# Optimization experiments

Hardware: AMD Instinct MI355X
Metric: run time of the kernel (lower is better)

The kernel has to match this reference:

```python
import jax, jax.numpy as jnp
import numpy as np

B, C, H, W = 8, 512, 64, 64
C8 = C // 8


def setup_inputs() -> dict:
    key = jax.random.key(0)
    ks = jax.random.split(key, 9)
    s = 1.0 / np.sqrt(C)
    return {
        "view1": jax.random.normal(ks[0], (B, C, H, W), jnp.float32),
        "view2": jax.random.normal(ks[1], (B, C, H, W), jnp.float32),
        "Wq": jax.random.normal(ks[2], (C8, C), jnp.float32) * s,
        "bq": jax.random.normal(ks[3], (C8,), jnp.float32) * 0.01,
        "Wk": jax.random.normal(ks[4], (C8, C), jnp.float32) * s,
        "bk": jax.random.normal(ks[5], (C8,), jnp.float32) * 0.01,
        "Wv": jax.random.normal(ks[6], (C, C), jnp.float32) * s,
        "bv": jax.random.normal(ks[7], (C,), jnp.float32) * 0.01,
        "gamma": jnp.array([0.5], jnp.float32),  # nn.Parameter(zeros(1)) in torch; nonzero here for nontrivial output
    }


def reference(view1, view2, Wq, bq, Wk, bk, Wv, bv, gamma):
    b, c, h, w = view1.shape
    n = h * w
    # 1x1 convs == per-pixel linear over channel dim
    q = jnp.einsum("bchw,oc->bohw", view1, Wq) + bq[None, :, None, None]
    k = jnp.einsum("bchw,oc->bohw", view2, Wk) + bk[None, :, None, None]
    v = jnp.einsum("bchw,oc->bohw", view2, Wv) + bv[None, :, None, None]
    q = q.reshape(b, -1, n).transpose(0, 2, 1)  # (B, N, C/8)
    k = k.reshape(b, -1, n)                      # (B, C/8, N)
    v = v.reshape(b, c, n)                       # (B, C, N)
    # no scaling, matching the original module
    attn = jax.nn.softmax(jnp.einsum("bnd,bdm->bnm", q, k), axis=-1)  # (B, N, N)
    out = jnp.einsum("bcn,bmn->bcm", v, attn).reshape(b, c, h, w)
    return gamma[0] * out + view1
```

## Files before the change

### kernel.cpp

```cpp
#include <hip/hip_runtime.h>

#define NB 8
#define NC 512
#define NPIX 4096
#define LOG2E 1.44269504088896340736f
#define C0TERM 28.853900817779268f

typedef __attribute__((ext_vector_type(4))) float f32x4;
typedef __attribute__((ext_vector_type(8))) short bf16x8;
typedef __attribute__((ext_vector_type(4))) unsigned short u16x4;

static __device__ __forceinline__ short f2bf(float f){
    union { float f; unsigned u; } v; v.f = f;
    unsigned r = v.u + 0x7fffu + ((v.u >> 16) & 1u);
    return (short)(r >> 16);
}

static __device__ __forceinline__ void gload16(const void* g, void* l){
    __builtin_amdgcn_global_load_lds(
        (const __attribute__((address_space(1))) char*)g,
        (__attribute__((address_space(3))) char*)l, 16, 0, 0);
}

__global__ void k_wconv(const float* __restrict__ wq, const float* __restrict__ wk,
                        const float* __restrict__ wv,
                        short* __restrict__ wqb, short* __restrict__ wkb,
                        short* __restrict__ wvb){
    int i = blockIdx.x * 256 + threadIdx.x;
    if (i < 64*NC){ wqb[i] = f2bf(wq[i]); wkb[i] = f2bf(wk[i]); }
    if (i < NC*NC){ wvb[i] = f2bf(wv[i]); }
}

__global__ __launch_bounds__(256) void k_projq(const float* __restrict__ X,
                                               const short* __restrict__ W,
                                               const float* __restrict__ bias,
                                               short* __restrict__ out){
    const int b = blockIdx.y;
    const int wv = threadIdx.x >> 6;
    const int lane = threadIdx.x & 63;
    const int g = lane >> 4, c16 = lane & 15;
    const int n0w = blockIdx.x * 64 + wv * 16;
    const float* Xb = X + (size_t)b * NC * NPIX;

    f32x4 acc[4];
#pragma unroll
    for (int f = 0; f < 4; ++f) acc[f] = (f32x4){0.f,0.f,0.f,0.f};

    for (int c0 = 0; c0 < NC; c0 += 32){
        bf16x8 a;
#pragma unroll
        for (int j = 0; j < 8; ++j)
            a[j] = f2bf(Xb[(size_t)(c0 + 8*g + j) * NPIX + n0w + c16]);
#pragma unroll
        for (int f = 0; f < 4; ++f){
            bf16x8 bfr = *(const bf16x8*)(W + (size_t)(f*16 + c16) * NC + c0 + 8*g);
            acc[f] = __builtin_amdgcn_mfma_f32_16x16x32_bf16(a, bfr, acc[f], 0, 0, 0);
        }
    }
#pragma unroll
    for (int f = 0; f < 4; ++f){
        int o = f*16 + c16;
        float bo = bias[o];
#pragma unroll
        for (int i = 0; i < 4; ++i)
            out[((size_t)b*NPIX + n0w + 4*g + i)*64 + o] = f2bf(acc[f][i] + bo);
    }
}

__global__ __launch_bounds__(256) void k_trans(const float* __restrict__ X,
                                               short* __restrict__ Xt){
    __shared__ __align__(16) short T[64][72];
    const int n0 = blockIdx.x * 64;
    const int c0 = blockIdx.y * 64;
    const int b  = blockIdx.z;
    const int t  = threadIdx.x;
    {
        const int cl = t >> 2;
        const int nq = (t & 3) * 16;
        const float* src = X + ((size_t)b*NC + c0 + cl)*NPIX + n0 + nq;
#pragma unroll
        for (int q = 0; q < 4; ++q){
            f32x4 v = *(const f32x4*)(src + q*4);
#pragma unroll
            for (int i = 0; i < 4; ++i)
                T[nq + q*4 + i][cl] = f2bf(v[i]);
        }
    }
    __syncthreads();
    {
        const int n  = t >> 2;
        const int cs = (t & 3) * 16;
        short* dst = Xt + ((size_t)b*NPIX + n0 + n)*NC + c0 + cs;
        *(f32x4*)dst       = *(const f32x4*)&T[n][cs];
        *(f32x4*)(dst + 8) = *(const f32x4*)&T[n][cs + 8];
    }
}

__global__ __launch_bounds__(256) void k_projv(const short* __restrict__ Xt,
                                               const short* __restrict__ W,
                                               const float* __restrict__ bias,
                                               short* __restrict__ vout){
    const int o0 = blockIdx.x * 128;
    const int n0 = blockIdx.y * 128;
    const int b  = blockIdx.z;
    const int wv = threadIdx.x >> 6;
    const int lane = threadIdx.x & 63;
    const int g = lane >> 4, c16 = lane & 15;
    const int wo = wv & 1, wn = wv >> 1;

    const short* Xb = Xt + ((size_t)b*NPIX + n0 + wn*64)*NC;
    const short* Wb = W + (size_t)(o0 + wo*64)*NC;

    f32x4 acc[4][4];
#pragma unroll
    for (int nf = 0; nf < 4; ++nf)
#pragma unroll
        for (int of = 0; of < 4; ++of) acc[nf][of] = (f32x4){0.f,0.f,0.f,0.f};

    for (int c0 = 0; c0 < NC; c0 += 32){
        bf16x8 af[4], bf_[4];
#pragma unroll
        for (int f = 0; f < 4; ++f){
            af[f]  = *(const bf16x8*)(Xb + (size_t)(f*16 + c16)*NC + c0 + 8*g);
            bf_[f] = *(const bf16x8*)(Wb + (size_t)(f*16 + c16)*NC + c0 + 8*g);
        }
#pragma unroll
        for (int nf = 0; nf < 4; ++nf)
#pragma unroll
            for (int of = 0; of < 4; ++of)
                acc[nf][of] = __builtin_amdgcn_mfma_f32_16x16x32_bf16(af[nf], bf_[of], acc[nf][of], 0,0,0);
    }

#pragma unroll
    for (int of = 0; of < 4; ++of){
        int o = o0 + wo*64 + of*16 + c16;
        float bo = bias[o];
#pragma unroll
        for (int nf = 0; nf < 4; ++nf){
            int n = n0 + wn*64 + nf*16 + 4*g;
            u16x4 pk;
#pragma unroll
            for (int i = 0; i < 4; ++i) pk[i] = (unsigned short)f2bf(acc[nf][of][i] + bo);
            *(u16x4*)(vout + ((size_t)b*NC + o)*NPIX + n) = pk;
        }
    }
}

__global__ __launch_bounds__(256) void k_projk(const short* __restrict__ Xt,
                                               const short* __restrict__ W,
                                               const float* __restrict__ bias,
                                               short* __restrict__ kout){
    const int n0 = blockIdx.x * 256;
    const int b  = blockIdx.y;
    const int wv = threadIdx.x >> 6;
    const int lane = threadIdx.x & 63;
    const int g = lane >> 4, c16 = lane & 15;

    const short* Xb = Xt + ((size_t)b*NPIX + n0 + wv*64)*NC;

    f32x4 acc[4][4];
#pragma unroll
    for (int of = 0; of < 4; ++of)
#pragma unroll
        for (int nf = 0; nf < 4; ++nf) acc[of][nf] = (f32x4){0.f,0.f,0.f,0.f};

    for (int c0 = 0; c0 < NC; c0 += 32){
        bf16x8 af[4], bf_[4];
#pragma unroll
        for (int f = 0; f < 4; ++f){
            af[f]  = *(const bf16x8*)(W + (size_t)(f*16 + c16)*NC + c0 + 8*g);
            bf_[f] = *(const bf16x8*)(Xb + (size_t)(f*16 + c16)*NC + c0 + 8*g);
        }
#pragma unroll
        for (int of = 0; of < 4; ++of)
#pragma unroll
            for (int nf = 0; nf < 4; ++nf)
                acc[of][nf] = __builtin_amdgcn_mfma_f32_16x16x32_bf16(af[of], bf_[nf], acc[of][nf], 0,0,0);
    }

#pragma unroll
    for (int nf = 0; nf < 4; ++nf){
        int n = n0 + wv*64 + nf*16 + c16;
#pragma unroll
        for (int of = 0; of < 4; ++of){
            int o = of*16 + 4*g;
            u16x4 pk;
#pragma unroll
            for (int i = 0; i < 4; ++i) pk[i] = (unsigned short)f2bf(acc[of][nf][i] + bias[o+i]);
            *(u16x4*)(kout + ((size_t)b*NPIX + n)*64 + o) = pk;
        }
    }
}

__global__ __launch_bounds__(256) void k_projkv(const float* __restrict__ X,
                                                const short* __restrict__ Wv_,
                                                const float* __restrict__ bv_,
                                                const short* __restrict__ Wk_,
                                                const float* __restrict__ bk_,
                                                short* __restrict__ vout,
                                                short* __restrict__ kout){
    const int b = blockIdx.y;
    const int wv = threadIdx.x >> 6;
    const int lane = threadIdx.x & 63;
    const int g = lane >> 4, c16 = lane & 15;
    const int n0w = blockIdx.x * 32 + (wv & 1) * 16;
    const int oh = wv >> 1;
    const int o0v = oh * 256;
    const int o0k = oh * 32;
    const float* Xb = X + (size_t)b * NC * NPIX;

    f32x4 accv[16], acck[2];
#pragma unroll
    for (int f = 0; f < 16; ++f) accv[f] = (f32x4){0.f,0.f,0.f,0.f};
#pragma unroll
    for (int f = 0; f < 2;  ++f) acck[f] = (f32x4){0.f,0.f,0.f,0.f};

    for (int c0 = 0; c0 < NC; c0 += 32){
        bf16x8 a;
#pragma unroll
        for (int j = 0; j < 8; ++j)
            a[j] = f2bf(Xb[(size_t)(c0 + 8*g + j) * NPIX + n0w + c16]);
#pragma unroll
        for (int f = 0; f < 16; ++f){
            bf16x8 bfr = *(const bf16x8*)(Wv_ + (size_t)(o0v + f*16 + c16) * NC + c0 + 8*g);
            accv[f] = __builtin_amdgcn_mfma_f32_16x16x32_bf16(a, bfr, accv[f], 0, 0, 0);
        }
#pragma unroll
        for (int f = 0; f < 2; ++f){
            bf16x8 bfr = *(const bf16x8*)(Wk_ + (size_t)(o0k + f*16 + c16) * NC + c0 + 8*g);
            acck[f] = __builtin_amdgcn_mfma_f32_16x16x32_bf16(a, bfr, acck[f], 0, 0, 0);
        }
    }
#pragma unroll
    for (int f = 0; f < 16; ++f){
        int o = o0v + f*16 + c16;
        float bo = bv_[o];
        u16x4 pk;
#pragma unroll
        for (int i = 0; i < 4; ++i) pk[i] = (unsigned short)f2bf(accv[f][i] + bo);
        *(u16x4*)(vout + ((size_t)b*NC + o)*NPIX + n0w + 4*g) = pk;
    }
#pragma unroll
    for (int f = 0; f < 2; ++f){
        int o = o0k + f*16 + c16;
        float bo = bk_[o];
#pragma unroll
        for (int i = 0; i < 4; ++i)
            kout[((size_t)b*NPIX + n0w + 4*g + i)*64 + o] = f2bf(acck[f][i] + bo);
    }
}

__global__ __launch_bounds__(256) void k_qk(const short* __restrict__ qb,
                                            const short* __restrict__ kb,
                                            short* __restrict__ P,
                                            float* __restrict__ Lpart,
                                            int b0){
    __shared__ __align__(16) short Pt[64*256];
    const int m0 = blockIdx.x * 64;
    const int n0 = blockIdx.y * 256;
    const int bz = blockIdx.z;
    const int b  = b0 + bz;
    const int wv = threadIdx.x >> 6;
    const int lane = threadIdx.x & 63;
    const int g = lane >> 4, c16 = lane & 15;
    const int nsub = wv * 64;

    bf16x8 qf[4][2];
#pragma unroll
    for (int mf = 0; mf < 4; ++mf)
#pragma unroll
        for (int kk = 0; kk < 2; ++kk)
            qf[mf][kk] = *(const bf16x8*)(qb + ((size_t)b*NPIX + m0 + mf*16 + c16)*64 + kk*32 + 8*g);

    float lsum[4] = {0.f,0.f,0.f,0.f};
    char* Ptb = (char*)Pt;

#pragma unroll
    for (int nf = 0; nf < 4; ++nf){
        bf16x8 kf0 = *(const bf16x8*)(kb + ((size_t)b*NPIX + n0 + nsub + nf*16 + c16)*64 + 8*g);
        bf16x8 kf1 = *(const bf16x8*)(kb + ((size_t)b*NPIX + n0 + nsub + nf*16 + c16)*64 + 32 + 8*g);
#pragma unroll
        for (int mf = 0; mf < 4; ++mf){
            f32x4 s = (f32x4){0.f,0.f,0.f,0.f};
            s = __builtin_amdgcn_mfma_f32_16x16x32_bf16(kf0, qf[mf][0], s, 0,0,0);
            s = __builtin_amdgcn_mfma_f32_16x16x32_bf16(kf1, qf[mf][1], s, 0,0,0);
            u16x4 pk;
#pragma unroll
            for (int i = 0; i < 4; ++i){
                float p = exp2f(fmaf(s[i], LOG2E, -C0TERM));
                lsum[mf] += p;
                pk[i] = (unsigned short)f2bf(p);
            }
            int m = mf*16 + c16;
            int ncol = nsub + nf*16 + 4*g;
            *(u16x4*)(Ptb + m*512 + ((2*ncol) ^ ((m&7)<<4))) = pk;
        }
    }
    __syncthreads();

    {
        char* Pgb = (char*)(P + ((size_t)bz*NPIX + m0)*NPIX + n0);
        const int chunk = threadIdx.x & 31;
        const int row8  = threadIdx.x >> 5;
#pragma unroll
        for (int p = 0; p < 8; ++p){
            int row = p*8 + row8;
            f32x4 v = *(const f32x4*)(Ptb + row*512 + ((chunk*16) ^ ((row&7)<<4)));
            *(f32x4*)(Pgb + (size_t)row*(NPIX*2) + chunk*16) = v;
        }
    }

#pragma unroll
    for (int mf = 0; mf < 4; ++mf){
        lsum[mf] += __shfl_xor(lsum[mf], 16);
        lsum[mf] += __shfl_xor(lsum[mf], 32);
    }
    if (lane < 16){
        size_t base = ((size_t)bz*64 + blockIdx.y*4 + wv)*NPIX + m0 + lane;
#pragma unroll
        for (int mf = 0; mf < 4; ++mf)
            Lpart[base + mf*16] = lsum[mf];
    }
}

__global__ __launch_bounds__(256) void k_lred(const float* __restrict__ Lpart,
                                              const float* __restrict__ gamma,
                                              float* __restrict__ scale){
    int idx = blockIdx.x * 256 + threadIdx.x;
    int bz = idx >> 12, m = idx & 4095;
    float s = 0.f;
    for (int sl = 0; sl < 64; ++sl)
        s += Lpart[((size_t)bz*64 + sl)*NPIX + m];
    scale[idx] = gamma[0] / s;
}

__global__ __launch_bounds__(256) void k_pv(const short* __restrict__ vb,
                                            const short* __restrict__ P,
                                            const float* __restrict__ scale,
                                            const float* __restrict__ view1,
                                            float* __restrict__ out,
                                            int b0){
    __shared__ __align__(16) short At[2][128*64];
    __shared__ __align__(16) short Bt[2][128*64];
    const int p  = blockIdx.x + 4*blockIdx.y;
    const int mt = (p & 7) | (((p >> 5) & 3) << 3);
    const int ct = (p >> 3) & 3;
    const int c0 = ct * 128;
    const int m0 = mt * 128;
    const int bz = blockIdx.z;
    const int b  = b0 + bz;
    const int wv = threadIdx.x >> 6;
    const int lane = threadIdx.x & 63;
    const int g = lane >> 4, c16 = lane & 15;
    const int wc = wv & 1, wm = wv >> 1;
    const int lrow = lane >> 3;
    const int srcg = (lane & 7) ^ lrow;
    const int swz  = (c16 & 7) << 4;

    const char* Vg = (const char*)(vb + ((size_t)b*NC + c0)*NPIX);
    const char* Pg = (const char*)(P + ((size_t)bz*NPIX + m0)*NPIX);

    f32x4 acc[4][4];
#pragma unroll
    for (int cf = 0; cf < 4; ++cf)
#pragma unroll
        for (int mf = 0; mf < 4; ++mf) acc[cf][mf] = (f32x4){0.f,0.f,0.f,0.f};

    auto stage = [&](int buf, int t){
        size_t nbyte = (size_t)t * 64 * 2;
#pragma unroll
        for (int j = 0; j < 4; ++j){
            int r0 = wv*32 + j*8;
            int row = r0 + lrow;
            gload16(Vg + (size_t)row*(NPIX*2) + nbyte + srcg*16, (char*)&At[buf][0] + r0*128);
            gload16(Pg + (size_t)row*(NPIX*2) + nbyte + srcg*16, (char*)&Bt[buf][0] + r0*128);
        }
    };

    stage(0, 0);
    __syncthreads();

    for (int t = 0; t < 64; ++t){
        int buf = t & 1;
        if (t < 63) stage(buf ^ 1, t + 1);
        const char* A  = (const char*)&At[buf][0];
        const char* Bp = (const char*)&Bt[buf][0];
#pragma unroll
        for (int kk = 0; kk < 2; ++kk){
            bf16x8 af[4], bfm[4];
#pragma unroll
            for (int f = 0; f < 4; ++f){
                af[f]  = *(const bf16x8*)(A  + (wc*64 + f*16 + c16)*128 + ((kk*64 + g*16) ^ swz));
                bfm[f] = *(const bf16x8*)(Bp + (wm*64 + f*16 + c16)*128 + ((kk*64 + g*16) ^ swz));
            }
#pragma unroll
            for (int cf = 0; cf < 4; ++cf)
#pragma unroll
                for (int mf = 0; mf < 4; ++mf)
                    acc[cf][mf] = __builtin_amdgcn_mfma_f32_16x16x32_bf16(af[cf], bfm[mf], acc[cf][mf], 0,0,0);
        }
        __syncthreads();
    }

    float sc[4];
#pragma unroll
    for (int mf = 0; mf < 4; ++mf)
        sc[mf] = scale[(size_t)bz*NPIX + m0 + wm*64 + mf*16 + c16];
#pragma unroll
    for (int cf = 0; cf < 4; ++cf){
#pragma unroll
        for (int mf = 0; mf < 4; ++mf){
            int m = m0 + wm*64 + mf*16 + c16;
#pragma unroll
            for (int i = 0; i < 4; ++i){
                int c = c0 + wc*64 + cf*16 + 4*g + i;
                size_t idx = ((size_t)b*NC + c)*NPIX + m;
                out[idx] = sc[mf]*acc[cf][mf][i] + view1[idx];
            }
        }
    }
}

__global__ __launch_bounds__(512, 2) void k_attn(const short* __restrict__ qb,
                                                 const short* __restrict__ kb,
                                                 const short* __restrict__ vb,
                                                 const float* __restrict__ view1,
                                                 const float* __restrict__ gamma,
                                                 float* __restrict__ out){
    __shared__ __align__(16) short P[2][64*64];
    __shared__ float Lred[128];

    const int bid = blockIdx.x;
    const int b  = bid & 7;
    const int m0 = (bid >> 3) * 64;
    const int wv = threadIdx.x >> 6;
    const int lane = threadIdx.x & 63;
    const int g = lane >> 4, c16 = lane & 15;
    const int msubA = (wv & 3) * 16;
    const int nhalf = wv >> 2;
    const int c0w = wv * 64;

    const short* qrow = qb + ((size_t)b*NPIX + m0 + msubA + c16)*64 + 8*g;
    bf16x8 qa0 = *(const bf16x8*)qrow;
    bf16x8 qa1 = *(const bf16x8*)(qrow + 32);

    const size_t kbase = (size_t)b * NPIX * 64;
    const int mrow = msubA + c16;
    const int swz = (mrow & 7) << 4;
    float Lacc = 0.f;

    f32x4 acc[4][4];
#pragma unroll
    for (int f = 0; f < 4; ++f)
#pragma unroll
        for (int cf = 0; cf < 4; ++cf) acc[f][cf] = (f32x4){0.f,0.f,0.f,0.f};

    char* Pb0 = (char*)&P[0][0];
    char* Pb1 = (char*)&P[1][0];

    bf16x8 vrA[8], vrB[8], krA[4], krB[4];

    auto loadK = [&](int t, bf16x8 (&kr)[4]){
        const short* kp = kb + kbase + (size_t)(t*64 + nhalf*32 + c16)*64 + 8*g;
        kr[0] = *(const bf16x8*)kp;
        kr[1] = *(const bf16x8*)(kp + 32);
        kr[2] = *(const bf16x8*)(kp + 16*64);
        kr[3] = *(const bf16x8*)(kp + 16*64 + 32);
    };
    auto loadV = [&](int t, bf16x8 (&vr)[8]){
#pragma unroll
        for (int h = 0; h < 2; ++h)
#pragma unroll
            for (int cf = 0; cf < 4; ++cf)
                vr[h*4+cf] = *(const bf16x8*)(vb + ((size_t)b*NC + c0w + cf*16 + c16)*NPIX
                                              + t*64 + h*32 + 8*g);
    };

    auto compA = [&](bf16x8 kA, bf16x8 kB, int fn, char* pb){
        f32x4 s = (f32x4){0.f,0.f,0.f,0.f};
        s = __builtin_amdgcn_mfma_f32_16x16x32_bf16(kA, qa0, s, 0,0,0);
        s = __builtin_amdgcn_mfma_f32_16x16x32_bf16(kB, qa1, s, 0,0,0);
        u16x4 pk;
#pragma unroll
        for (int i = 0; i < 4; ++i){
            float p = exp2f(fmaf(s[i], LOG2E, -C0TERM));
            Lacc += p;
            pk[i] = (unsigned short)f2bf(p);
        }
        int nrel0 = nhalf*32 + fn*16 + 4*g;
        *(u16x4*)(pb + mrow*128 + ((2*nrel0) ^ swz)) = pk;
    };

    auto phaseB = [&](const char* pc, const bf16x8 (&vr)[8]){
#pragma unroll
        for (int h = 0; h < 2; ++h){
            bf16x8 pa[4];
#pragma unroll
            for (int f = 0; f < 4; ++f){
                int row = f*16 + c16;
                pa[f] = *(const bf16x8*)(pc + row*128 + ((h*64 + g*16) ^ ((row&7)<<4)));
            }
#pragma unroll
            for (int cf = 0; cf < 4; ++cf)
#pragma unroll
                for (int f = 0; f < 4; ++f)
                    acc[f][cf] = __builtin_amdgcn_mfma_f32_16x16x32_bf16(pa[f], vr[h*4+cf], acc[f][cf], 0,0,0);
        }
    };

    auto iter = [&](int t, char* bufA, const char* bufB,
                    const bf16x8 (&vcur)[8], bf16x8 (&vnext)[8],
                    const bf16x8 (&kcur)[4], bf16x8 (&knext)[4]){
        loadV(t+1, vnext);
        loadK(t+2 < 64 ? t+2 : 63, knext);
        __builtin_amdgcn_s_setprio(1);
        phaseB(bufB, vcur);
        __builtin_amdgcn_s_setprio(0);
        compA(kcur[0], kcur[1], 0, bufA);
        compA(kcur[2], kcur[3], 1, bufA);
        asm volatile("s_waitcnt lgkmcnt(0)" ::: "memory");
        __builtin_amdgcn_s_barrier();
    };

    loadV(0, vrA);
    loadK(0, krA);
    loadK(1, krB);
    compA(krA[0], krA[1], 0, Pb0);
    compA(krA[2], krA[3], 1, Pb0);
    asm volatile("s_waitcnt lgkmcnt(0)" ::: "memory");
    __builtin_amdgcn_s_barrier();

    for (int t2 = 0; t2 < 31; ++t2){
        iter(2*t2,     Pb1, Pb0, vrA, vrB, krB, krA);
        iter(2*t2 + 1, Pb0, Pb1, vrB, vrA, krA, krB);
    }
    iter(62, Pb1, Pb0, vrA, vrB, krB, krA);
    __builtin_amdgcn_s_setprio(1);
    phaseB(Pb1, vrB);
    __builtin_amdgcn_s_setprio(0);

    Lacc += __shfl_xor(Lacc, 16);
    Lacc += __shfl_xor(Lacc, 32);
    if (lane < 16) Lred[nhalf*64 + msubA + lane] = Lacc;
    __syncthreads();

    float gm = gamma[0];
#pragma unroll
    for (int f = 0; f < 4; ++f){
        float sc[4];
#pragma unroll
        for (int i = 0; i < 4; ++i){
            int r = f*16 + 4*g + i;
            float Ls = Lred[r] + Lred[64 + r];
            sc[i] = gm / Ls;
        }
#pragma unroll
        for (int cf = 0; cf < 4; ++cf){
            int c = c0w + cf*16 + c16;
            size_t base = ((size_t)b*NC + c)*NPIX + m0 + f*16 + 4*g;
            f32x4 v1 = *(const f32x4*)(view1 + base);
            f32x4 r;
#pragma unroll
            for (int i = 0; i < 4; ++i) r[i] = sc[i]*acc[f][cf][i] + v1[i];
            *(f32x4*)(out + base) = r;
        }
    }
}

extern "C" void kernel_launch(void* const* d_in, const int* in_sizes, int n_in,
                              void* d_out, int out_size, void* d_ws, size_t ws_size,
                              hipStream_t stream){
    const float* view1 = (const float*)d_in[0];
    const float* view2 = (const float*)d_in[1];
    const float* Wq    = (const float*)d_in[2];
    const float* bq    = (const float*)d_in[3];
    const float* Wk    = (const float*)d_in[4];
    const float* bk    = (const float*)d_in[5];
    const float* Wv    = (const float*)d_in[6];
    const float* bv    = (const float*)d_in[7];
    const float* gamma = (const float*)d_in[8];
    float* out = (float*)d_out;

    char* ws = (char*)d_ws;
    short* qbuf = (short*)(ws);
    short* kbuf = (short*)(ws + (size_t)4*1024*1024);
    short* vbuf = (short*)(ws + (size_t)8*1024*1024);
    short* wqb  = (short*)(ws + (size_t)40*1024*1024);
    short* wkb  = (short*)(ws + (size_t)40*1024*1024 + 64*1024);
    short* wvb  = (short*)(ws + (size_t)40*1024*1024 + 128*1024);
    float* scl  = (float*)(ws + (size_t)41*1024*1024);
    float* Lpart= (float*)(ws + (size_t)42*1024*1024);
    short* Pbuf = (short*)(ws + (size_t)50*1024*1024);
    short* X2t  = Pbuf;

    const size_t FIXED = (size_t)50*1024*1024;
    const size_t PPB   = (size_t)NPIX*NPIX*2;
    int avail = 0;
    if (ws_size > FIXED){
        size_t nn = (ws_size - FIXED) / PPB;
        avail = nn > 8 ? 8 : (int)nn;
    }
    int nbc = (avail >= 8) ? 8 : (avail >= 4) ? 4 : (avail >= 2) ? 2 : avail;

    hipLaunchKernelGGL(k_wconv, dim3(1024), dim3(256), 0, stream, Wq, Wk, Wv, wqb, wkb, wvb);
    hipLaunchKernelGGL(k_projq,  dim3(64, 8),  dim3(256), 0, stream, view1, wqb, bq, qbuf);

    if (nbc >= 1){
        hipLaunchKernelGGL(k_trans, dim3(64, 8, 8), dim3(256), 0, stream, view2, X2t);
        hipLaunchKernelGGL(k_projv, dim3(4, 32, 8), dim3(256), 0, stream, X2t, wvb, bv, vbuf);
        hipLaunchKernelGGL(k_projk, dim3(16, 8),    dim3(256), 0, stream, X2t, wkb, bk, kbuf);
        for (int b0 = 0; b0 < NB; b0 += nbc){
            int nb = (NB - b0 < nbc) ? (NB - b0) : nbc;
            hipLaunchKernelGGL(k_qk,   dim3(64, 16, nb), dim3(256), 0, stream, qbuf, kbuf, Pbuf, Lpart, b0);
            hipLaunchKernelGGL(k_lred, dim3(nb*16),      dim3(256), 0, stream, Lpart, gamma, scl);
            hipLaunchKernelGGL(k_pv,   dim3(4, 32, nb),  dim3(256), 0, stream, vbuf, Pbuf, scl, view1, out, b0);
        }
    } else {
        hipLaunchKernelGGL(k_projkv, dim3(128, 8), dim3(256), 0, stream, view2, wvb, bv, wkb, bk, vbuf, kbuf);
        hipLaunchKernelGGL(k_attn, dim3(512), dim3(512), 0, stream, qbuf, kbuf, vbuf, view1, gamma, out);
    }
}
```

Before: 413.0 us.

## Unroll PV loop with explicit vmcnt waits and route Q projection via transpose

The PV kernel's double-buffered K loop is restructured into a 2-step unrolled pipeline. Each step uses explicit s_waitcnt vmcnt, raw barriers, sched_barriers and setprio around the MFMA block, so the next tile's loads stay in flight while the current tile is computed, in place of a full __syncthreads drain. Separately, when workspace allows, view1 is transposed to bf16 and the Q projection reuses the k_projk kernel instead of k_projq. This adds a transpose pass and depends on the hand-tuned vmcnt counts (8 outstanding loads) being correct.

```diff
diff --git a/kernel.cpp b/kernel.cpp
--- a/kernel.cpp
+++ b/kernel.cpp
@@ -21,6 +21,11 @@
         (const __attribute__((address_space(1))) char*)g,
         (__attribute__((address_space(3))) char*)l, 16, 0, 0);
 }
+
+#define VW8 asm volatile("s_waitcnt vmcnt(8)" ::: "memory")
+#define VW0 asm volatile("s_waitcnt vmcnt(0)" ::: "memory")
+#define BAR __builtin_amdgcn_s_barrier()
+#define SB0 __builtin_amdgcn_sched_barrier(0)
 
 __global__ void k_wconv(const float* __restrict__ wq, const float* __restrict__ wk,
                         const float* __restrict__ wv,
@@ -377,12 +382,7 @@
         }
     };
 
-    stage(0, 0);
-    __syncthreads();
-
-    for (int t = 0; t < 64; ++t){
-        int buf = t & 1;
-        if (t < 63) stage(buf ^ 1, t + 1);
+    auto kstep = [&](int buf){
         const char* A  = (const char*)&At[buf][0];
         const char* Bp = (const char*)&Bt[buf][0];
 #pragma unroll
@@ -393,14 +393,33 @@
                 af[f]  = *(const bf16x8*)(A  + (wc*64 + f*16 + c16)*128 + ((kk*64 + g*16) ^ swz));
                 bfm[f] = *(const bf16x8*)(Bp + (wm*64 + f*16 + c16)*128 + ((kk*64 + g*16) ^ swz));
             }
+            __builtin_amdgcn_s_setprio(1);
 #pragma unroll
             for (int cf = 0; cf < 4; ++cf)
 #pragma unroll
                 for (int mf = 0; mf < 4; ++mf)
                     acc[cf][mf] = __builtin_amdgcn_mfma_f32_16x16x32_bf16(af[cf], bfm[mf], acc[cf][mf], 0,0,0);
-        }
-        __syncthreads();
-    }
+            __builtin_amdgcn_s_setprio(0);
+        }
+    };
+
+    stage(0, 0);
+    stage(1, 1);
+
+    for (int t2 = 0; t2 < 31; ++t2){
+        VW8; BAR; SB0;
+        kstep(0);
+        BAR;
+        stage(0, 2*t2 + 2);
+        VW8; BAR; SB0;
+        kstep(1);
+        BAR;
+        stage(1, 2*t2 + 3);
+    }
+    VW8; BAR; SB0;
+    kstep(0);
+    VW0; BAR; SB0;
+    kstep(1);
 
     float sc[4];
 #pragma unroll
@@ -592,6 +611,7 @@
     float* Lpart= (float*)(ws + (size_t)42*1024*1024);
     short* Pbuf = (short*)(ws + (size_t)50*1024*1024);
     short* X2t  = Pbuf;
+    short* X1t  = Pbuf + (size_t)16*1024*1024;
 
     const size_t FIXED = (size_t)50*1024*1024;
     const size_t PPB   = (size_t)NPIX*NPIX*2;
@@ -603,12 +623,17 @@
     int nbc = (avail >= 8) ? 8 : (avail >= 4) ? 4 : (avail >= 2) ? 2 : avail;
 
     hipLaunchKernelGGL(k_wconv, dim3(1024), dim3(256), 0, stream, Wq, Wk, Wv, wqb, wkb, wvb);
-    hipLaunchKernelGGL(k_projq,  dim3(64, 8),  dim3(256), 0, stream, view1, wqb, bq, qbuf);
 
     if (nbc >= 1){
         hipLaunchKernelGGL(k_trans, dim3(64, 8, 8), dim3(256), 0, stream, view2, X2t);
         hipLaunchKernelGGL(k_projv, dim3(4, 32, 8), dim3(256), 0, stream, X2t, wvb, bv, vbuf);
         hipLaunchKernelGGL(k_projk, dim3(16, 8),    dim3(256), 0, stream, X2t, wkb, bk, kbuf);
+        if (nbc >= 2){
+            hipLaunchKernelGGL(k_trans, dim3(64, 8, 8), dim3(256), 0, stream, view1, X1t);
+            hipLaunchKernelGGL(k_projk, dim3(16, 8),    dim3(256), 0, stream, X1t, wqb, bq, qbuf);
+        } else {
+            hipLaunchKernelGGL(k_projq, dim3(64, 8), dim3(256), 0, stream, view1, wqb, bq, qbuf);
+        }
         for (int b0 = 0; b0 < NB; b0 += nbc){
             int nb = (NB - b0 < nbc) ? (NB - b0) : nbc;
             hipLaunchKernelGGL(k_qk,   dim3(64, 16, nb), dim3(256), 0, stream, qbuf, kbuf, Pbuf, Lpart, b0);
@@ -616,6 +641,7 @@
             hipLaunchKernelGGL(k_pv,   dim3(4, 32, nb),  dim3(256), 0, stream, vbuf, Pbuf, scl, view1, out, b0);
         }
     } else {
+        hipLaunchKernelGGL(k_projq,  dim3(64, 8),  dim3(256), 0, stream, view1, wqb, bq, qbuf);
         hipLaunchKernelGGL(k_projkv, dim3(128, 8), dim3(256), 0, stream, view2, wvb, bv, wkb, bk, vbuf, kbuf);
         hipLaunchKernelGGL(k_attn, dim3(512), dim3(512), 0, stream, qbuf, kbuf, vbuf, view1, gamma, out);
     }
```

Measured after the change: 421.6 us. 1.02x slower.

## Load PV operands directly to registers and compute Q projection via transpose path

Applied to the files above, without the earlier changes.

The P·V kernel stops staging V and P tiles through LDS with async global-to-LDS copies and barriers. Each wave now loads its MFMA fragments straight from global memory into registers, double-buffered in registers across k-steps. Separately, the Q projection now transposes view1 and reuses the k_projk kernel with the Q weights when enough workspace exists. The direct loads give up data sharing between waves through LDS, so global and L2 traffic go up, while the barriers and LDS round trips go away.

```diff
diff --git a/kernel.cpp b/kernel.cpp
--- a/kernel.cpp
+++ b/kernel.cpp
@@ -14,12 +14,6 @@
     union { float f; unsigned u; } v; v.f = f;
     unsigned r = v.u + 0x7fffu + ((v.u >> 16) & 1u);
     return (short)(r >> 16);
-}
-
-static __device__ __forceinline__ void gload16(const void* g, void* l){
-    __builtin_amdgcn_global_load_lds(
-        (const __attribute__((address_space(1))) char*)g,
-        (__attribute__((address_space(3))) char*)l, 16, 0, 0);
 }
 
 __global__ void k_wconv(const float* __restrict__ wq, const float* __restrict__ wk,
@@ -340,8 +334,6 @@
                                             const float* __restrict__ view1,
                                             float* __restrict__ out,
                                             int b0){
-    __shared__ __align__(16) short At[2][128*64];
-    __shared__ __align__(16) short Bt[2][128*64];
     const int p  = blockIdx.x + 4*blockIdx.y;
     const int mt = (p & 7) | (((p >> 5) & 3) << 3);
     const int ct = (p >> 3) & 3;
@@ -353,12 +345,14 @@
     const int lane = threadIdx.x & 63;
     const int g = lane >> 4, c16 = lane & 15;
     const int wc = wv & 1, wm = wv >> 1;
-    const int lrow = lane >> 3;
-    const int srcg = (lane & 7) ^ lrow;
-    const int swz  = (c16 & 7) << 4;
-
-    const char* Vg = (const char*)(vb + ((size_t)b*NC + c0)*NPIX);
-    const char* Pg = (const char*)(P + ((size_t)bz*NPIX + m0)*NPIX);
+
+    const short* Vp[4];
+    const short* Pp[4];
+#pragma unroll
+    for (int f = 0; f < 4; ++f){
+        Vp[f] = vb + ((size_t)b*NC + c0 + wc*64 + f*16 + c16)*NPIX + 8*g;
+        Pp[f] = P  + ((size_t)bz*NPIX + m0 + wm*64 + f*16 + c16)*NPIX + 8*g;
+    }
 
     f32x4 acc[4][4];
 #pragma unroll
@@ -366,40 +360,45 @@
 #pragma unroll
         for (int mf = 0; mf < 4; ++mf) acc[cf][mf] = (f32x4){0.f,0.f,0.f,0.f};
 
-    auto stage = [&](int buf, int t){
-        size_t nbyte = (size_t)t * 64 * 2;
-#pragma unroll
-        for (int j = 0; j < 4; ++j){
-            int r0 = wv*32 + j*8;
-            int row = r0 + lrow;
-            gload16(Vg + (size_t)row*(NPIX*2) + nbyte + srcg*16, (char*)&At[buf][0] + r0*128);
-            gload16(Pg + (size_t)row*(NPIX*2) + nbyte + srcg*16, (char*)&Bt[buf][0] + r0*128);
-        }
+    bf16x8 vA[4], pA[4], vB[4], pB[4];
+#pragma unroll
+    for (int f = 0; f < 4; ++f){
+        vA[f] = *(const bf16x8*)(Vp[f]);
+        pA[f] = *(const bf16x8*)(Pp[f]);
+    }
+
+    auto comp = [&](const bf16x8 (&vf)[4], const bf16x8 (&pf)[4]){
+#pragma unroll
+        for (int cf = 0; cf < 4; ++cf)
+#pragma unroll
+            for (int mf = 0; mf < 4; ++mf)
+                acc[cf][mf] = __builtin_amdgcn_mfma_f32_16x16x32_bf16(vf[cf], pf[mf], acc[cf][mf], 0,0,0);
     };
 
-    stage(0, 0);
-    __syncthreads();
-
-    for (int t = 0; t < 64; ++t){
-        int buf = t & 1;
-        if (t < 63) stage(buf ^ 1, t + 1);
-        const char* A  = (const char*)&At[buf][0];
-        const char* Bp = (const char*)&Bt[buf][0];
-#pragma unroll
-        for (int kk = 0; kk < 2; ++kk){
-            bf16x8 af[4], bfm[4];
-#pragma unroll
-            for (int f = 0; f < 4; ++f){
-                af[f]  = *(const bf16x8*)(A  + (wc*64 + f*16 + c16)*128 + ((kk*64 + g*16) ^ swz));
-                bfm[f] = *(const bf16x8*)(Bp + (wm*64 + f*16 + c16)*128 + ((kk*64 + g*16) ^ swz));
-            }
-#pragma unroll
-            for (int cf = 0; cf < 4; ++cf)
-#pragma unroll
-                for (int mf = 0; mf < 4; ++mf)
-                    acc[cf][mf] = __builtin_amdgcn_mfma_f32_16x16x32_bf16(af[cf], bfm[mf], acc[cf][mf], 0,0,0);
-        }
-        __syncthreads();
+    for (int t2 = 0; t2 < 63; ++t2){
+        const size_t ob = (size_t)(2*t2 + 1) * 32;
+#pragma unroll
+        for (int f = 0; f < 4; ++f){
+            vB[f] = *(const bf16x8*)(Vp[f] + ob);
+            pB[f] = *(const bf16x8*)(Pp[f] + ob);
+        }
+        comp(vA, pA);
+#pragma unroll
+        for (int f = 0; f < 4; ++f){
+            vA[f] = *(const bf16x8*)(Vp[f] + ob + 32);
+            pA[f] = *(const bf16x8*)(Pp[f] + ob + 32);
+        }
+        comp(vB, pB);
+    }
+    {
+        const size_t ob = (size_t)127 * 32;
+#pragma unroll
+        for (int f = 0; f < 4; ++f){
+            vB[f] = *(const bf16x8*)(Vp[f] + ob);
+            pB[f] = *(const bf16x8*)(Pp[f] + ob);
+        }
+        comp(vA, pA);
+        comp(vB, pB);
     }
 
     float sc[4];
@@ -592,6 +591,7 @@
     float* Lpart= (float*)(ws + (size_t)42*1024*1024);
     short* Pbuf = (short*)(ws + (size_t)50*1024*1024);
     short* X2t  = Pbuf;
+    short* X1t  = Pbuf + (size_t)16*1024*1024;
 
     const size_t FIXED = (size_t)50*1024*1024;
     const size_t PPB   = (size_t)NPIX*NPIX*2;
@@ -603,12 +603,17 @@
     int nbc = (avail >= 8) ? 8 : (avail >= 4) ? 4 : (avail >= 2) ? 2 : avail;
 
     hipLaunchKernelGGL(k_wconv, dim3(1024), dim3(256), 0, stream, Wq, Wk, Wv, wqb, wkb, wvb);
-    hipLaunchKernelGGL(k_projq,  dim3(64, 8),  dim3(256), 0, stream, view1, wqb, bq, qbuf);
 
     if (nbc >= 1){
         hipLaunchKernelGGL(k_trans, dim3(64, 8, 8), dim3(256), 0, stream, view2, X2t);
         hipLaunchKernelGGL(k_projv, dim3(4, 32, 8), dim3(256), 0, stream, X2t, wvb, bv, vbuf);
         hipLaunchKernelGGL(k_projk, dim3(16, 8),    dim3(256), 0, stream, X2t, wkb, bk, kbuf);
+        if (nbc >= 2){
+            hipLaunchKernelGGL(k_trans, dim3(64, 8, 8), dim3(256), 0, stream, view1, X1t);
+            hipLaunchKernelGGL(k_projk, dim3(16, 8),    dim3(256), 0, stream, X1t, wqb, bq, qbuf);
+        } else {
+            hipLaunchKernelGGL(k_projq, dim3(64, 8), dim3(256), 0, stream, view1, wqb, bq, qbuf);
+        }
         for (int b0 = 0; b0 < NB; b0 += nbc){
             int nb = (NB - b0 < nbc) ? (NB - b0) : nbc;
             hipLaunchKernelGGL(k_qk,   dim3(64, 16, nb), dim3(256), 0, stream, qbuf, kbuf, Pbuf, Lpart, b0);
@@ -616,6 +621,7 @@
             hipLaunchKernelGGL(k_pv,   dim3(4, 32, nb),  dim3(256), 0, stream, vbuf, Pbuf, scl, view1, out, b0);
         }
     } else {
+        hipLaunchKernelGGL(k_projq,  dim3(64, 8),  dim3(256), 0, stream, view1, wqb, bq, qbuf);
         hipLaunchKernelGGL(k_projkv, dim3(128, 8), dim3(256), 0, stream, view2, wvb, bv, wkb, bk, vbuf, kbuf);
         hipLaunchKernelGGL(k_attn, dim3(512), dim3(512), 0, stream, qbuf, kbuf, vbuf, view1, gamma, out);
     }
```

New measurement: 727.0 us. +76.0%, slower.
